# Optimization experiments

Hardware: AMD Instinct MI355X
Metric: run time of the kernel (lower is better)

The kernel has to match this reference:

```python
import jax, jax.numpy as jnp
from jax import lax
import numpy as np

B, H, T = 16, 1024, 1500
K = 3               # conv kernel size
MAX_TOK = 192       # max_decode_tokens (static padded token dim)
TEMP = 0.35
LLW = 0.25          # length_loss_weight
EPS = 1e-6


def setup_inputs() -> dict:
    key = jax.random.key(0)
    ks = jax.random.split(key, 8)
    encoder_outputs = jax.random.normal(ks[0], (B, H, T), dtype=jnp.float32)
    encoder_lengths = jax.random.randint(ks[1], (B,), 0, T)
    target_token_lengths = jax.random.randint(ks[2], (B,), 0, MAX_TOK)
    conv_w = jax.random.normal(ks[3], (H, H, K), dtype=jnp.float32) * 0.02  # OIH
    conv_b = jax.random.normal(ks[4], (H,), dtype=jnp.float32) * 0.02
    proj_w = jax.random.normal(ks[5], (H,), dtype=jnp.float32) * 0.02      # Linear(H,1)
    proj_b = jax.random.normal(ks[6], (), dtype=jnp.float32) * 0.02
    return {
        "encoder_outputs": encoder_outputs,
        "encoder_lengths": encoder_lengths,
        "target_token_lengths": target_token_lengths,
        "conv_w": conv_w,
        "conv_b": conv_b,
        "proj_w": proj_w,
        "proj_b": proj_b,
    }


def reference(encoder_outputs, encoder_lengths, target_token_lengths,
              conv_w, conv_b, proj_w, proj_b):
    b, h, t = encoder_outputs.shape
    dt = encoder_outputs.dtype

    # temporal conv (same padding), channel-first
    conv = lax.conv_general_dilated(
        encoder_outputs, conv_w, window_strides=(1,), padding="SAME",
        dimension_numbers=("NCH", "OIH", "NCH")) + conv_b[None, :, None]
    conv_feat = conv.transpose(0, 2, 1)  # [B,T,H]

    # softplus(Linear(silu(conv_feat))) + 1e-4  -> raw weights [B,T]
    raw = jax.nn.softplus(
        jnp.einsum("bth,h->bt", jax.nn.silu(conv_feat), proj_w) + proj_b) + 1e-4

    time_mask = (jnp.arange(t)[None, :] < encoder_lengths[:, None]).astype(dt)
    raw = raw * time_mask
    raw_mass = raw.sum(axis=1)  # [B]

    tok_len = jnp.clip(target_token_lengths, 1, MAX_TOK)
    alignment_loss = jnp.mean(jnp.abs(raw_mass - tok_len.astype(dt))) * LLW

    # vectorized (masked) version of the per-sample loop, padded to MAX_TOK
    scale = tok_len.astype(dt) / jnp.maximum(raw_mass, EPS)          # [B]
    sw = raw * scale[:, None]                                        # scaled weights [B,T]
    centers = jnp.cumsum(sw, axis=1) - 0.5 * sw                      # [B,T]
    token_centers = jnp.arange(MAX_TOK, dtype=dt) + 0.5              # [K]
    dist = centers[:, :, None] - token_centers[None, None, :]        # [B,T,K]
    assign = jnp.exp(-(dist * dist) / (2.0 * TEMP * TEMP)) * sw[:, :, None]
    assign = assign / jnp.maximum(assign.sum(axis=1, keepdims=True), EPS)
    tok_mask = (jnp.arange(MAX_TOK)[None, :] < tok_len[:, None]).astype(dt)
    assign = assign * tok_mask[:, None, :]

    features = encoder_outputs.transpose(0, 2, 1)                    # [B,T,H]
    acoustic_tokens = jnp.einsum("btk,bth->bkh", assign, features)   # [B,MAX_TOK,H]
    return acoustic_tokens, tok_len, alignment_loss
```

## Files before the change

### kernel.cpp

```cpp
#include <hip/hip_runtime.h>
#include <stdint.h>

#define B_ 16
#define H_ 1024
#define T_ 1500
#define MAXTOK 192
#define NCOL (B_*T_)
#define TCOLS 1536
#define KDIM (3*H_)
#define TPADX 1544
#define TPK  1536
#define SPAD 1504
#define INV2T2 (1.0f/(2.0f*0.35f*0.35f))
#define LOSS_IDX (B_*MAXTOK*H_ + B_)
#define TOK_BASE (B_*MAXTOK*H_)

typedef __bf16 bf16x8 __attribute__((ext_vector_type(8)));
typedef float  f32x4  __attribute__((ext_vector_type(4)));
typedef __attribute__((address_space(3))) unsigned int       lds_u32;
typedef __attribute__((address_space(1))) const unsigned int g_u32;

__device__ __forceinline__ void gload_lds16(const void* g, void* l) {
    __builtin_amdgcn_global_load_lds((g_u32*)g, (lds_u32*)l, 16, 0, 0);
}

__device__ __forceinline__ unsigned short f2bf(float f) {
    unsigned int u = __float_as_uint(f);
    unsigned int r = (u + 0x7FFFu + ((u >> 16) & 1u)) >> 16;
    return (unsigned short)r;
}

__global__ void init_kernel(float* rawacc, float* out, unsigned short* Xt) {
    int idx = blockIdx.x * blockDim.x + threadIdx.x;
    if (idx < NCOL) { rawacc[idx] = 0.f; return; }
    if (idx == NCOL) { out[LOSS_IDX] = 0.f; return; }
    int j = idx - (NCOL + 1);
    if (j < B_*5632) {
        int b = j / 5632, r = j - b*5632;
        long halfoff = (long)b*TPADX*1024 +
                       ((r < 128) ? (long)r*8 : (1501L*1024 + (long)(r-128)*8));
        uint4 z = make_uint4(0u,0u,0u,0u);
        *(uint4*)&Xt[halfoff] = z;
    }
}

__global__ void precast_w(const float* __restrict__ cw, unsigned short* __restrict__ Ar) {
    int idx = blockIdx.x * blockDim.x + threadIdx.x;
    if (idx >= H_*KDIM) return;
    int h = idx / KDIM, rem = idx - h*KDIM;
    int k = rem >> 10, i = rem & 1023;
    Ar[idx] = f2bf(cw[h*KDIM + i*3 + k]);
}

__global__ __launch_bounds__(256) void transpose_x(
    const float* __restrict__ x, unsigned short* __restrict__ Xt,
    unsigned short* __restrict__ XtT)
{
    __shared__ float tile[64][68];
    int b = blockIdx.z;
    int t0 = blockIdx.x * 64;
    int i0 = blockIdx.y * 64;
    int tx = threadIdx.x & 15;
    int ty = threadIdx.x >> 4;

    #pragma unroll
    for (int p = 0; p < 4; ++p) {
        int i = p*16 + ty;
        int t = t0 + tx*4;
        float4 v = make_float4(0.f, 0.f, 0.f, 0.f);
        if (t + 3 < T_) v = *(const float4*)&x[((long)b*H_ + i0 + i)*T_ + t];
        *(float4*)&tile[i][tx*4] = v;
        ushort4 u;
        u.x = f2bf(v.x); u.y = f2bf(v.y); u.z = f2bf(v.z); u.w = f2bf(v.w);
        *(ushort4*)&XtT[((long)b*H_ + i0 + i)*TPK + t] = u;
    }
    __syncthreads();
    #pragma unroll
    for (int p = 0; p < 4; ++p) {
        int t = p*16 + ty;
        if (t0 + t < T_) {
            ushort4 u;
            u.x = f2bf(tile[tx*4 + 0][t]);
            u.y = f2bf(tile[tx*4 + 1][t]);
            u.z = f2bf(tile[tx*4 + 2][t]);
            u.w = f2bf(tile[tx*4 + 3][t]);
            *(ushort4*)&Xt[((long)b*TPADX + t0 + t + 1)*1024 + i0 + tx*4] = u;
        }
    }
}

__global__ __launch_bounds__(256) void conv_gemm(
    const unsigned short* __restrict__ Ar, const unsigned short* __restrict__ Xt,
    const float* __restrict__ conv_b, const float* __restrict__ proj_w,
    float* __restrict__ rawacc)
{
    __shared__ unsigned short As[128*64];
    __shared__ unsigned short Bs[136*64];
    __shared__ float colsum[128];
    int bid = blockIdx.x;
    int xcd = bid & 7;
    int j = bid >> 3;
    int h_idx = j / 24;
    int g = j - h_idx*24;
    int n_idx = xcd*24 + g;
    int bb = n_idx / 12;
    int t0 = (n_idx - bb*12) * 128;
    int h0 = h_idx * 128;

    int tid = threadIdx.x;
    int w = tid >> 6, lane = tid & 63;
    int lrow = lane >> 3;
    int lcol = ((lane & 7) ^ lrow) * 8;

    const unsigned short* aptr = Ar + (long)(h0 + w*32 + lrow) * KDIM + lcol;
    const unsigned short* bX   = Xt + ((long)bb*TPADX + t0 + lrow) * 1024 + lcol;
    unsigned short* lAs = &As[(w*32)*64];

    f32x4 acc[4][4];
    f32x4 zero = {0.f, 0.f, 0.f, 0.f};
    #pragma unroll
    for (int a = 0; a < 4; ++a)
        #pragma unroll
        for (int c = 0; c < 4; ++c) acc[a][c] = zero;

    int wm = w >> 1, wn = w & 1;
    int quad = lane >> 4, l16 = lane & 15;
    int sw8a = (l16 & 7) * 8;

    for (int c = 0; c < 16; ++c) {
        __syncthreads();
        for (int s = w; s < 17; s += 4)
            gload_lds16(bX + (long)s*8*1024 + c*64, &Bs[s*8*64]);
        #pragma unroll
        for (int kk = 0; kk < 3; ++kk) {
            if (kk) __syncthreads();
            #pragma unroll
            for (int i = 0; i < 4; ++i)
                gload_lds16(aptr + (long)i*8*KDIM + kk*1024 + c*64, lAs + i*8*64);
            __syncthreads();
            int sw8b = ((l16 + kk) & 7) * 8;
            #pragma unroll
            for (int ks = 0; ks < 2; ++ks) {
                int base = ks*32 + quad*8;
                int cofa = base ^ sw8a;
                int cofb = base ^ sw8b;
                bf16x8 af[4], bfr[4];
                #pragma unroll
                for (int mi = 0; mi < 4; ++mi)
                    af[mi] = *(const bf16x8*)&As[(wm*64 + mi*16 + l16)*64 + cofa];
                #pragma unroll
                for (int ni = 0; ni < 4; ++ni)
                    bfr[ni] = *(const bf16x8*)&Bs[(wn*64 + ni*16 + l16 + kk)*64 + cofb];
                #pragma unroll
                for (int mi = 0; mi < 4; ++mi)
                    #pragma unroll
                    for (int ni = 0; ni < 4; ++ni)
                        acc[mi][ni] = __builtin_amdgcn_mfma_f32_16x16x32_bf16(
                            af[mi], bfr[ni], acc[mi][ni], 0, 0, 0);
            }
        }
    }

    if (tid < 128) colsum[tid] = 0.f;
    __syncthreads();
    float cp[4] = {0.f, 0.f, 0.f, 0.f};
    #pragma unroll
    for (int mi = 0; mi < 4; ++mi) {
        #pragma unroll
        for (int r = 0; r < 4; ++r) {
            int h = h0 + wm*64 + mi*16 + quad*4 + r;
            float bias = conv_b[h], wgt = proj_w[h];
            #pragma unroll
            for (int ni = 0; ni < 4; ++ni) {
                float v = acc[mi][ni][r] + bias;
                float s = v / (1.f + expf(-v));
                cp[ni] += s * wgt;
            }
        }
    }
    #pragma unroll
    for (int ni = 0; ni < 4; ++ni)
        atomicAdd(&colsum[wn*64 + ni*16 + l16], cp[ni]);
    __syncthreads();
    if (tid < 128) {
        int t = t0 + tid;
        if (t < T_) atomicAdd(&rawacc[bb*T_ + t], colsum[tid]);
    }
}

__global__ void scan_kernel(const float* __restrict__ rawacc, const float* __restrict__ proj_b,
                            const int* __restrict__ elen, const int* __restrict__ tgt,
                            float* __restrict__ sw, float* __restrict__ centers,
                            float* __restrict__ out) {
    int b = blockIdx.x;
    int lane = threadIdx.x;
    float pb = proj_b[0];
    int el = elen[b];
    const float* ra = rawacc + b*T_;

    float m = 0.f;
    for (int t = lane; t < T_; t += 64) {
        float xv = ra[t] + pb;
        float sp = (xv > 20.f) ? xv : log1pf(expf(xv));
        m += (t < el) ? sp + 1e-4f : 0.f;
    }
    #pragma unroll
    for (int off = 32; off > 0; off >>= 1) m += __shfl_down(m, off);
    float mass = __shfl(m, 0);
    int tok = min(max(tgt[b], 1), MAXTOK);
    if (lane == 0) {
        atomicAdd(&out[LOSS_IDX], fabsf(mass - (float)tok) * (0.25f / (float)B_));
        out[TOK_BASE + b] = (float)tok;
    }
    float scale = (float)tok / fmaxf(mass, 1e-6f);
    float running = 0.f;
    for (int t0 = 0; t0 < T_; t0 += 64) {
        int t = t0 + lane;
        float v = 0.f;
        if (t < T_) {
            float xv = ra[t] + pb;
            float sp = (xv > 20.f) ? xv : log1pf(expf(xv));
            v = ((t < el) ? sp + 1e-4f : 0.f) * scale;
        }
        float s = v;
        #pragma unroll
        for (int d = 1; d < 64; d <<= 1) {
            float u = __shfl_up(s, d);
            if (lane >= d) s += u;
        }
        if (t < T_) {
            sw[b*SPAD + t] = v;
            centers[b*SPAD + t] = running + s - 0.5f*v;
        }
        running += __shfl(s, 63);
    }
}

__global__ __launch_bounds__(256) void denom_an(
    const float* __restrict__ sw, const float* __restrict__ cen,
    const int* __restrict__ tgt, unsigned short* __restrict__ An)
{
    __shared__ float ebuf[TPK];
    __shared__ float wsum[4];
    __shared__ float dsh;
    int kk = blockIdx.x;
    int b  = blockIdx.y;
    int tid = threadIdx.x;
    int tok = min(max(tgt[b], 1), MAXTOK);
    bool live = (kk < tok);
    float tc = kk + 0.5f;

    float lsum = 0.f;
    for (int t = tid; t < TPK; t += 256) {
        float e = 0.f;
        if (live && t < T_) {
            float d = cen[b*SPAD + t] - tc;
            e = expf(-d*d*INV2T2) * sw[b*SPAD + t];
        }
        ebuf[t] = e;
        lsum += e;
    }
    #pragma unroll
    for (int off = 32; off > 0; off >>= 1) lsum += __shfl_down(lsum, off);
    if ((tid & 63) == 0) wsum[tid >> 6] = lsum;
    __syncthreads();
    if (tid == 0) dsh = 1.f / fmaxf(wsum[0] + wsum[1] + wsum[2] + wsum[3], 1e-6f);
    __syncthreads();
    float invden = dsh;

    unsigned short* dst = An + ((long)b*MAXTOK + kk) * TPK;
    for (int q = tid; q < TPK/4; q += 256) {
        ushort4 u;
        u.x = f2bf(ebuf[q*4 + 0] * invden);
        u.y = f2bf(ebuf[q*4 + 1] * invden);
        u.z = f2bf(ebuf[q*4 + 2] * invden);
        u.w = f2bf(ebuf[q*4 + 3] * invden);
        *(ushort4*)&dst[q*4] = u;
    }
}

__global__ __launch_bounds__(256) void einsum_gemm(
    const unsigned short* __restrict__ An, const unsigned short* __restrict__ XtT,
    const int* __restrict__ tgt, float* __restrict__ out)
{
    __shared__ unsigned short As2[64*64];
    __shared__ unsigned short Bs2[128*64];
    int b  = blockIdx.z;
    int kk0 = blockIdx.x * 64;
    int h0  = blockIdx.y * 128;
    int tid = threadIdx.x;
    int tok = min(max(tgt[b], 1), MAXTOK);

    if (kk0 >= tok) {
        f32x4 z = {0.f, 0.f, 0.f, 0.f};
        #pragma unroll
        for (int i = 0; i < 8; ++i) {
            int lin = i*256 + tid;
            int row = lin >> 5, c4 = lin & 31;
            *(f32x4*)&out[((long)b*MAXTOK + kk0 + row)*H_ + h0 + c4*4] = z;
        }
        return;
    }

    int w = tid >> 6, lane = tid & 63;
    int lrow = lane >> 3;
    int lcol = ((lane & 7) ^ lrow) * 8;

    const unsigned short* aptr = An  + ((long)b*MAXTOK + kk0 + w*16 + lrow) * TPK + lcol;
    const unsigned short* bptr = XtT + ((long)b*H_    + h0  + w*32 + lrow) * TPK + lcol;
    unsigned short* lAs = &As2[(w*16)*64];
    unsigned short* lBs = &Bs2[(w*32)*64];

    f32x4 acc[2][4];
    f32x4 zero = {0.f, 0.f, 0.f, 0.f};
    #pragma unroll
    for (int a = 0; a < 2; ++a)
        #pragma unroll
        for (int c = 0; c < 4; ++c) acc[a][c] = zero;

    int wm = w >> 1, wn = w & 1;
    int quad = lane >> 4, l16 = lane & 15;
    int sw8 = (l16 & 7) * 8;

    for (int kt = 0; kt < TPK/64; ++kt) {
        __syncthreads();
        #pragma unroll
        for (int i = 0; i < 2; ++i)
            gload_lds16(aptr + (long)i*8*TPK + kt*64, lAs + i*8*64);
        #pragma unroll
        for (int i = 0; i < 4; ++i)
            gload_lds16(bptr + (long)i*8*TPK + kt*64, lBs + i*8*64);
        __syncthreads();
        #pragma unroll
        for (int ks = 0; ks < 2; ++ks) {
            int cofs = (ks*32 + quad*8) ^ sw8;
            bf16x8 af[2], bfr[4];
            #pragma unroll
            for (int mi = 0; mi < 2; ++mi)
                af[mi] = *(const bf16x8*)&As2[(wm*32 + mi*16 + l16)*64 + cofs];
            #pragma unroll
            for (int ni = 0; ni < 4; ++ni)
                bfr[ni] = *(const bf16x8*)&Bs2[(wn*64 + ni*16 + l16)*64 + cofs];
            #pragma unroll
            for (int mi = 0; mi < 2; ++mi)
                #pragma unroll
                for (int ni = 0; ni < 4; ++ni)
                    acc[mi][ni] = __builtin_amdgcn_mfma_f32_16x16x32_bf16(
                        af[mi], bfr[ni], acc[mi][ni], 0, 0, 0);
        }
    }

    #pragma unroll
    for (int mi = 0; mi < 2; ++mi) {
        int kk = kk0 + wm*32 + mi*16 + quad*4;
        #pragma unroll
        for (int ni = 0; ni < 4; ++ni) {
            int h = h0 + wn*64 + ni*16 + l16;
            long base = ((long)b*MAXTOK + kk)*H_ + h;
            #pragma unroll
            for (int r = 0; r < 4; ++r)
                out[base + (long)r*H_] = acc[mi][ni][r];
        }
    }
}

extern "C" void kernel_launch(void* const* d_in, const int* in_sizes, int n_in,
                              void* d_out, int out_size, void* d_ws, size_t ws_size,
                              hipStream_t stream)
{
    const float* x      = (const float*)d_in[0];
    const int*   elen   = (const int*)d_in[1];
    const int*   tlen   = (const int*)d_in[2];
    const float* conv_w = (const float*)d_in[3];
    const float* conv_b = (const float*)d_in[4];
    const float* proj_w = (const float*)d_in[5];
    const float* proj_b = (const float*)d_in[6];
    float* out = (float*)d_out;

    unsigned short* Xt  = (unsigned short*)d_ws;
    unsigned short* Ar  = Xt  + (size_t)B_*TPADX*1024;
    unsigned short* XtT = Ar  + (size_t)H_*KDIM;
    unsigned short* An  = XtT + (size_t)B_*H_*TPK;
    float* fbase  = (float*)(An + (size_t)B_*MAXTOK*TPK);
    float* rawacc = fbase;
    float* swv    = rawacc + NCOL;
    float* cen    = swv + B_*SPAD;

    int init_n = NCOL + 1 + B_*5632;
    init_kernel<<<(init_n + 255)/256, 256, 0, stream>>>(rawacc, out, Xt);
    precast_w<<<(H_*KDIM + 255)/256, 256, 0, stream>>>(conv_w, Ar);
    transpose_x<<<dim3(24, 16, 16), 256, 0, stream>>>(x, Xt, XtT);
    conv_gemm<<<1536, 256, 0, stream>>>(Ar, Xt, conv_b, proj_w, rawacc);
    scan_kernel<<<B_, 64, 0, stream>>>(rawacc, proj_b, elen, tlen, swv, cen, out);
    denom_an<<<dim3(MAXTOK, B_), 256, 0, stream>>>(swv, cen, tlen, An);
    einsum_gemm<<<dim3(3, 8, 16), 256, 0, stream>>>(An, XtT, tlen, out);
}
```

Before: 400.9 us.

## Load conv GEMM A fragments directly to registers with prefetch; merge prep kernels

The conv GEMM no longer stages the weight tile through LDS. Each wave loads its A fragments straight from global memory into registers, double-buffered across the three kernel taps, which removes two barriers per tap and frees LDS. The init and weight-precast kernels are merged into one launch. In exchange, A loads are now 16-byte scattered global reads with no sharing between waves, so register pressure and global traffic rise, and the latency of the first A load in each chunk is exposed.

```diff
diff --git a/kernel.cpp b/kernel.cpp
--- a/kernel.cpp
+++ b/kernel.cpp
@@ -6,7 +6,6 @@
 #define T_ 1500
 #define MAXTOK 192
 #define NCOL (B_*T_)
-#define TCOLS 1536
 #define KDIM (3*H_)
 #define TPADX 1544
 #define TPK  1536
@@ -30,8 +29,16 @@
     return (unsigned short)r;
 }
 
-__global__ void init_kernel(float* rawacc, float* out, unsigned short* Xt) {
+__global__ void prep_kernel(const float* __restrict__ cw, unsigned short* __restrict__ Ar,
+                            float* rawacc, float* out, unsigned short* Xt) {
     int idx = blockIdx.x * blockDim.x + threadIdx.x;
+    if (idx < H_*KDIM) {
+        int h = idx / KDIM, rem = idx - h*KDIM;
+        int k = rem >> 10, i = rem & 1023;
+        Ar[idx] = f2bf(cw[h*KDIM + i*3 + k]);
+        return;
+    }
+    idx -= H_*KDIM;
     if (idx < NCOL) { rawacc[idx] = 0.f; return; }
     if (idx == NCOL) { out[LOSS_IDX] = 0.f; return; }
     int j = idx - (NCOL + 1);
@@ -44,14 +51,6 @@
     }
 }
 
-__global__ void precast_w(const float* __restrict__ cw, unsigned short* __restrict__ Ar) {
-    int idx = blockIdx.x * blockDim.x + threadIdx.x;
-    if (idx >= H_*KDIM) return;
-    int h = idx / KDIM, rem = idx - h*KDIM;
-    int k = rem >> 10, i = rem & 1023;
-    Ar[idx] = f2bf(cw[h*KDIM + i*3 + k]);
-}
-
 __global__ __launch_bounds__(256) void transpose_x(
     const float* __restrict__ x, unsigned short* __restrict__ Xt,
     unsigned short* __restrict__ XtT)
@@ -94,7 +93,6 @@
     const float* __restrict__ conv_b, const float* __restrict__ proj_w,
     float* __restrict__ rawacc)
 {
-    __shared__ unsigned short As[128*64];
     __shared__ unsigned short Bs[136*64];
     __shared__ float colsum[128];
     int bid = blockIdx.x;
@@ -111,10 +109,11 @@
     int w = tid >> 6, lane = tid & 63;
     int lrow = lane >> 3;
     int lcol = ((lane & 7) ^ lrow) * 8;
-
-    const unsigned short* aptr = Ar + (long)(h0 + w*32 + lrow) * KDIM + lcol;
-    const unsigned short* bX   = Xt + ((long)bb*TPADX + t0 + lrow) * 1024 + lcol;
-    unsigned short* lAs = &As[(w*32)*64];
+    int wm = w >> 1, wn = w & 1;
+    int quad = lane >> 4, l16 = lane & 15;
+
+    const unsigned short* bX = Xt + ((long)bb*TPADX + t0 + lrow) * 1024 + lcol;
+    const unsigned short* aB = Ar + (long)(h0 + wm*64 + l16) * KDIM + quad*8;
 
     f32x4 acc[4][4];
     f32x4 zero = {0.f, 0.f, 0.f, 0.f};
@@ -123,31 +122,33 @@
         #pragma unroll
         for (int c = 0; c < 4; ++c) acc[a][c] = zero;
 
-    int wm = w >> 1, wn = w & 1;
-    int quad = lane >> 4, l16 = lane & 15;
-    int sw8a = (l16 & 7) * 8;
+    bf16x8 pf[2][4][2];
 
     for (int c = 0; c < 16; ++c) {
         __syncthreads();
         for (int s = w; s < 17; s += 4)
             gload_lds16(bX + (long)s*8*1024 + c*64, &Bs[s*8*64]);
         #pragma unroll
+        for (int mi = 0; mi < 4; ++mi)
+            #pragma unroll
+            for (int ks = 0; ks < 2; ++ks)
+                pf[0][mi][ks] = *(const bf16x8*)(aB + (long)mi*16*KDIM + c*64 + ks*32);
+        __syncthreads();
+        #pragma unroll
         for (int kk = 0; kk < 3; ++kk) {
-            if (kk) __syncthreads();
-            #pragma unroll
-            for (int i = 0; i < 4; ++i)
-                gload_lds16(aptr + (long)i*8*KDIM + kk*1024 + c*64, lAs + i*8*64);
-            __syncthreads();
-            int sw8b = ((l16 + kk) & 7) * 8;
-            #pragma unroll
-            for (int ks = 0; ks < 2; ++ks) {
-                int base = ks*32 + quad*8;
-                int cofa = base ^ sw8a;
-                int cofb = base ^ sw8b;
-                bf16x8 af[4], bfr[4];
+            if (kk < 2) {
                 #pragma unroll
                 for (int mi = 0; mi < 4; ++mi)
-                    af[mi] = *(const bf16x8*)&As[(wm*64 + mi*16 + l16)*64 + cofa];
+                    #pragma unroll
+                    for (int ks = 0; ks < 2; ++ks)
+                        pf[(kk+1)&1][mi][ks] = *(const bf16x8*)(
+                            aB + (long)mi*16*KDIM + (kk+1)*1024 + c*64 + ks*32);
+            }
+            int sw8b = ((l16 + kk) & 7) * 8;
+            #pragma unroll
+            for (int ks = 0; ks < 2; ++ks) {
+                int cofb = (ks*32 + quad*8) ^ sw8b;
+                bf16x8 bfr[4];
                 #pragma unroll
                 for (int ni = 0; ni < 4; ++ni)
                     bfr[ni] = *(const bf16x8*)&Bs[(wn*64 + ni*16 + l16 + kk)*64 + cofb];
@@ -156,7 +157,7 @@
                     #pragma unroll
                     for (int ni = 0; ni < 4; ++ni)
                         acc[mi][ni] = __builtin_amdgcn_mfma_f32_16x16x32_bf16(
-                            af[mi], bfr[ni], acc[mi][ni], 0, 0, 0);
+                            pf[kk&1][mi][ks], bfr[ni], acc[mi][ni], 0, 0, 0);
             }
         }
     }
@@ -386,9 +387,8 @@
     float* swv    = rawacc + NCOL;
     float* cen    = swv + B_*SPAD;
 
-    int init_n = NCOL + 1 + B_*5632;
-    init_kernel<<<(init_n + 255)/256, 256, 0, stream>>>(rawacc, out, Xt);
-    precast_w<<<(H_*KDIM + 255)/256, 256, 0, stream>>>(conv_w, Ar);
+    int prep_n = H_*KDIM + NCOL + 1 + B_*5632;
+    prep_kernel<<<(prep_n + 255)/256, 256, 0, stream>>>(conv_w, Ar, rawacc, out, Xt);
     transpose_x<<<dim3(24, 16, 16), 256, 0, stream>>>(x, Xt, XtT);
     conv_gemm<<<1536, 256, 0, stream>>>(Ar, Xt, conv_b, proj_w, rawacc);
     scan_kernel<<<B_, 64, 0, stream>>>(rawacc, proj_b, elen, tlen, swv, cen, out);
```

After: 540.8 us. +34.9%, slower.

## Merge prep kernels into one launch and load all three conv taps per chunk

Applied to the files above, without the earlier changes.

Combines the init, weight precast and input transpose kernels into a single stage kernel dispatched by block index, removing two kernel launches. In the conv GEMM, the A tiles for all three kernel taps are now loaded into LDS at once (tripling the As buffer), so each K chunk needs one barrier instead of three. This reduces synchronisation and launch overhead, but raises LDS use per block, which may lower occupancy.

```diff
diff --git a/kernel.cpp b/kernel.cpp
--- a/kernel.cpp
+++ b/kernel.cpp
@@ -6,7 +6,6 @@
 #define T_ 1500
 #define MAXTOK 192
 #define NCOL (B_*T_)
-#define TCOLS 1536
 #define KDIM (3*H_)
 #define TPADX 1544
 #define TPK  1536
@@ -14,6 +13,7 @@
 #define INV2T2 (1.0f/(2.0f*0.35f*0.35f))
 #define LOSS_IDX (B_*MAXTOK*H_ + B_)
 #define TOK_BASE (B_*MAXTOK*H_)
+#define TRBLK (24*16*16)
 
 typedef __bf16 bf16x8 __attribute__((ext_vector_type(8)));
 typedef float  f32x4  __attribute__((ext_vector_type(4)));
@@ -30,8 +30,54 @@
     return (unsigned short)r;
 }
 
-__global__ void init_kernel(float* rawacc, float* out, unsigned short* Xt) {
-    int idx = blockIdx.x * blockDim.x + threadIdx.x;
+__global__ __launch_bounds__(256) void stage_kernel(
+    const float* __restrict__ x, unsigned short* __restrict__ Xt,
+    unsigned short* __restrict__ XtT,
+    const float* __restrict__ cw, unsigned short* __restrict__ Ar,
+    float* rawacc, float* out)
+{
+    if (blockIdx.x < TRBLK) {
+        __shared__ float tile[64][68];
+        int bi = blockIdx.x;
+        int t0 = (bi % 24) * 64;
+        int i0 = ((bi / 24) & 15) * 64;
+        int b  = bi / 384;
+        int tx = threadIdx.x & 15;
+        int ty = threadIdx.x >> 4;
+        #pragma unroll
+        for (int p = 0; p < 4; ++p) {
+            int i = p*16 + ty;
+            int t = t0 + tx*4;
+            float4 v = make_float4(0.f, 0.f, 0.f, 0.f);
+            if (t + 3 < T_) v = *(const float4*)&x[((long)b*H_ + i0 + i)*T_ + t];
+            *(float4*)&tile[i][tx*4] = v;
+            ushort4 u;
+            u.x = f2bf(v.x); u.y = f2bf(v.y); u.z = f2bf(v.z); u.w = f2bf(v.w);
+            *(ushort4*)&XtT[((long)b*H_ + i0 + i)*TPK + t] = u;
+        }
+        __syncthreads();
+        #pragma unroll
+        for (int p = 0; p < 4; ++p) {
+            int t = p*16 + ty;
+            if (t0 + t < T_) {
+                ushort4 u;
+                u.x = f2bf(tile[tx*4 + 0][t]);
+                u.y = f2bf(tile[tx*4 + 1][t]);
+                u.z = f2bf(tile[tx*4 + 2][t]);
+                u.w = f2bf(tile[tx*4 + 3][t]);
+                *(ushort4*)&Xt[((long)b*TPADX + t0 + t + 1)*1024 + i0 + tx*4] = u;
+            }
+        }
+        return;
+    }
+    int idx = (blockIdx.x - TRBLK) * blockDim.x + threadIdx.x;
+    if (idx < H_*KDIM) {
+        int h = idx / KDIM, rem = idx - h*KDIM;
+        int k = rem >> 10, i = rem & 1023;
+        Ar[idx] = f2bf(cw[h*KDIM + i*3 + k]);
+        return;
+    }
+    idx -= H_*KDIM;
     if (idx < NCOL) { rawacc[idx] = 0.f; return; }
     if (idx == NCOL) { out[LOSS_IDX] = 0.f; return; }
     int j = idx - (NCOL + 1);
@@ -44,57 +90,12 @@
     }
 }
 
-__global__ void precast_w(const float* __restrict__ cw, unsigned short* __restrict__ Ar) {
-    int idx = blockIdx.x * blockDim.x + threadIdx.x;
-    if (idx >= H_*KDIM) return;
-    int h = idx / KDIM, rem = idx - h*KDIM;
-    int k = rem >> 10, i = rem & 1023;
-    Ar[idx] = f2bf(cw[h*KDIM + i*3 + k]);
-}
-
-__global__ __launch_bounds__(256) void transpose_x(
-    const float* __restrict__ x, unsigned short* __restrict__ Xt,
-    unsigned short* __restrict__ XtT)
-{
-    __shared__ float tile[64][68];
-    int b = blockIdx.z;
-    int t0 = blockIdx.x * 64;
-    int i0 = blockIdx.y * 64;
-    int tx = threadIdx.x & 15;
-    int ty = threadIdx.x >> 4;
-
-    #pragma unroll
-    for (int p = 0; p < 4; ++p) {
-        int i = p*16 + ty;
-        int t = t0 + tx*4;
-        float4 v = make_float4(0.f, 0.f, 0.f, 0.f);
-        if (t + 3 < T_) v = *(const float4*)&x[((long)b*H_ + i0 + i)*T_ + t];
-        *(float4*)&tile[i][tx*4] = v;
-        ushort4 u;
-        u.x = f2bf(v.x); u.y = f2bf(v.y); u.z = f2bf(v.z); u.w = f2bf(v.w);
-        *(ushort4*)&XtT[((long)b*H_ + i0 + i)*TPK + t] = u;
-    }
-    __syncthreads();
-    #pragma unroll
-    for (int p = 0; p < 4; ++p) {
-        int t = p*16 + ty;
-        if (t0 + t < T_) {
-            ushort4 u;
-            u.x = f2bf(tile[tx*4 + 0][t]);
-            u.y = f2bf(tile[tx*4 + 1][t]);
-            u.z = f2bf(tile[tx*4 + 2][t]);
-            u.w = f2bf(tile[tx*4 + 3][t]);
-            *(ushort4*)&Xt[((long)b*TPADX + t0 + t + 1)*1024 + i0 + tx*4] = u;
-        }
-    }
-}
-
 __global__ __launch_bounds__(256) void conv_gemm(
     const unsigned short* __restrict__ Ar, const unsigned short* __restrict__ Xt,
     const float* __restrict__ conv_b, const float* __restrict__ proj_w,
     float* __restrict__ rawacc)
 {
-    __shared__ unsigned short As[128*64];
+    __shared__ unsigned short As[3*128*64];
     __shared__ unsigned short Bs[136*64];
     __shared__ float colsum[128];
     int bid = blockIdx.x;
@@ -132,12 +133,14 @@
         for (int s = w; s < 17; s += 4)
             gload_lds16(bX + (long)s*8*1024 + c*64, &Bs[s*8*64]);
         #pragma unroll
+        for (int kk = 0; kk < 3; ++kk)
+            #pragma unroll
+            for (int i = 0; i < 4; ++i)
+                gload_lds16(aptr + (long)i*8*KDIM + kk*1024 + c*64,
+                            lAs + kk*8192 + i*8*64);
+        __syncthreads();
+        #pragma unroll
         for (int kk = 0; kk < 3; ++kk) {
-            if (kk) __syncthreads();
-            #pragma unroll
-            for (int i = 0; i < 4; ++i)
-                gload_lds16(aptr + (long)i*8*KDIM + kk*1024 + c*64, lAs + i*8*64);
-            __syncthreads();
             int sw8b = ((l16 + kk) & 7) * 8;
             #pragma unroll
             for (int ks = 0; ks < 2; ++ks) {
@@ -147,7 +150,7 @@
                 bf16x8 af[4], bfr[4];
                 #pragma unroll
                 for (int mi = 0; mi < 4; ++mi)
-                    af[mi] = *(const bf16x8*)&As[(wm*64 + mi*16 + l16)*64 + cofa];
+                    af[mi] = *(const bf16x8*)&As[kk*8192 + (wm*64 + mi*16 + l16)*64 + cofa];
                 #pragma unroll
                 for (int ni = 0; ni < 4; ++ni)
                     bfr[ni] = *(const bf16x8*)&Bs[(wn*64 + ni*16 + l16 + kk)*64 + cofb];
@@ -386,10 +389,9 @@
     float* swv    = rawacc + NCOL;
     float* cen    = swv + B_*SPAD;
 
-    int init_n = NCOL + 1 + B_*5632;
-    init_kernel<<<(init_n + 255)/256, 256, 0, stream>>>(rawacc, out, Xt);
-    precast_w<<<(H_*KDIM + 255)/256, 256, 0, stream>>>(conv_w, Ar);
-    transpose_x<<<dim3(24, 16, 16), 256, 0, stream>>>(x, Xt, XtT);
+    int prep_n = H_*KDIM + NCOL + 1 + B_*5632;
+    int grid = TRBLK + (prep_n + 255)/256;
+    stage_kernel<<<grid, 256, 0, stream>>>(x, Xt, XtT, conv_w, Ar, rawacc, out);
     conv_gemm<<<1536, 256, 0, stream>>>(Ar, Xt, conv_b, proj_w, rawacc);
     scan_kernel<<<B_, 64, 0, stream>>>(rawacc, proj_b, elen, tlen, swv, cen, out);
     denom_an<<<dim3(MAXTOK, B_), 256, 0, stream>>>(swv, cen, tlen, An);
```

Result: faster. 392.3 us (-2.1%).
